# Kernel tuning notes

Hardware: AMD Instinct MI355X
Metric: run time of the kernel (lower is better)

## Reference

```python
import jax, jax.numpy as jnp
import numpy as np

D = 512      # d_model
H = 8        # n_heads
HD = D // H  # head_dim
WIN = 128    # local window
CB = 8       # chunk base
NL = 3       # hierarchy levels
DFF = 1536
B, S = 4, 4096
EPS = 1e-6


def setup_inputs() -> dict:
    key = jax.random.key(0)
    ks = jax.random.split(key, 12)
    sd = 0.02
    inp = {
        'x': jax.random.normal(ks[0], (B, S, D), jnp.float32),
        'norm1_w': jnp.ones((D,), jnp.float32),
        'norm2_w': jnp.ones((D,), jnp.float32),
        'wq': jax.random.normal(ks[1], (D, D), jnp.float32) * sd,
        'wk': jax.random.normal(ks[2], (D, D), jnp.float32) * sd,
        'wv': jax.random.normal(ks[3], (D, D), jnp.float32) * sd,
        'wo': jax.random.normal(ks[4], (D, D), jnp.float32) * sd,
        'gamma': jnp.full((NL,), 0.1, jnp.float32),
        'w1': jax.random.normal(ks[5], (D, DFF), jnp.float32) * sd,
        'w2': jax.random.normal(ks[6], (D, DFF), jnp.float32) * sd,
        'w3': jax.random.normal(ks[7], (DFF, D), jnp.float32) * sd,
    }
    return inp


def rmsnorm(x, w):
    return x * jax.lax.rsqrt(jnp.mean(x * x, axis=-1, keepdims=True) + EPS) * w


def hier_attn(x, wq, wk, wv, wo, gamma):
    b, s, _ = x.shape
    scale = HD ** -0.5
    q = (x @ wq).reshape(b, s, H, HD).transpose(0, 2, 1, 3)  # (b,H,s,hd)
    k = (x @ wk).reshape(b, s, H, HD).transpose(0, 2, 1, 3)
    v = (x @ wv).reshape(b, s, H, HD).transpose(0, 2, 1, 3)

    nb = s // WIN
    qb = q.reshape(b, H, nb, WIN, HD)
    kp = jnp.concatenate([jnp.zeros_like(k[:, :, :WIN]), k], axis=2).reshape(b, H, nb + 1, WIN, HD)
    vp = jnp.concatenate([jnp.zeros_like(v[:, :, :WIN]), v], axis=2).reshape(b, H, nb + 1, WIN, HD)
    kw = jnp.concatenate([kp[:, :, :-1], kp[:, :, 1:]], axis=3)  # (b,H,nb,2W,hd)
    vw = jnp.concatenate([vp[:, :, :-1], vp[:, :, 1:]], axis=3)
    sc = jnp.einsum('bhnqd,bhnkd->bhnqk', qb, kw) * scale
    a_ = jnp.arange(WIN)[:, None]
    j_ = jnp.arange(2 * WIN)[None, :]
    base = (j_ > a_) & (j_ <= a_ + WIN)
    blk = (jnp.arange(nb)[:, None, None] > 0) | (j_ >= WIN)  # first block has no left half
    mask = base[None] & blk                                  # (nb,W,2W)
    sc = jnp.where(mask[None, None], sc, -1e9)
    out = jnp.einsum('bhnqk,bhnkd->bhnqd', jax.nn.softmax(sc, axis=-1), vw).reshape(b, H, s, HD)

    # ---- levels 1..NL: causal attention over mean-pooled chunk summaries ----
    pos = jnp.arange(s)
    for lvl in range(1, NL + 1):
        C = CB ** lvl
        nc = s // C
        kc = k.reshape(b, H, nc, C, HD).mean(axis=3)
        vc = v.reshape(b, H, nc, C, HD).mean(axis=3)
        sl = jnp.einsum('bhsd,bhcd->bhsc', q, kc) * scale
        m = jnp.arange(nc)[None, :] < (pos // C)[:, None]    # chunk strictly in the past
        sl = jnp.where(m[None, None], sl, -1e9)
        p = jax.nn.softmax(sl, axis=-1)
        p = p * m.any(axis=-1)[None, None, :, None]          # zero rows with no valid chunk
        out = out + gamma[lvl - 1] * jnp.einsum('bhsc,bhcd->bhsd', p, vc)

    return out.transpose(0, 2, 1, 3).reshape(b, s, D) @ wo


def swiglu(x, w1, w2, w3):
    return (jax.nn.silu(x @ w1) * (x @ w2)) @ w3


def reference(x, norm1_w, norm2_w, wq, wk, wv, wo, gamma, w1, w2, w3):
    h = x + hier_attn(rmsnorm(x, norm1_w), wq, wk, wv, wo, gamma)
    return h + swiglu(rmsnorm(h, norm2_w), w1, w2, w3)
```

## Files before the change

### kernel.cpp

```cpp
#include <hip/hip_runtime.h>
#include <stdint.h>

typedef unsigned short US;
typedef __attribute__((ext_vector_type(8))) short short8;
typedef __attribute__((ext_vector_type(8))) US us8;
typedef __attribute__((ext_vector_type(4))) float f32x4;
typedef __attribute__((ext_vector_type(4))) int i32x4;

#define DEV static __device__ __forceinline__

DEV US f2b(float f){
  uint32_t u = __builtin_bit_cast(uint32_t, f);
  return (US)((u + 0x7fffu + ((u >> 16) & 1u)) >> 16);
}
DEV US f2b_fast(float f){
  uint32_t u = __builtin_bit_cast(uint32_t, f);
  return (US)((u + 0x8000u) >> 16);
}
DEV float b2f(US s){
  return __builtin_bit_cast(float, (uint32_t)((uint32_t)s << 16));
}
DEV short8 ldsfrag(const US* p){
  return __builtin_bit_cast(short8, *(const i32x4*)p);
}
DEV f32x4 MFMA(short8 a, short8 b, f32x4 c){
  return __builtin_amdgcn_mfma_f32_16x16x32_bf16(a, b, c, 0, 0, 0);
}
DEV void async16(const US* g, US* l){
  __builtin_amdgcn_global_load_lds(
      (const __attribute__((address_space(1))) unsigned int*)(const void*)g,
      (__attribute__((address_space(3))) unsigned int*)(void*)l,
      16, 0, 0);
}

struct WcvtArgs {
  const float* src[7];
  US* dst[7];
  int R[7];
  int C[7];
};

__global__ __launch_bounds__(256) void wcvt(WcvtArgs a){
  int z = blockIdx.z;
  int R = a.R[z], C = a.C[z];
  int tc = blockIdx.x*32, tr = blockIdx.y*32;
  if (tc >= C || tr >= R) return;
  __shared__ float T[32][33];
  int tx = threadIdx.x & 31, ty = threadIdx.x >> 5;
  const float* s = a.src[z];
  #pragma unroll
  for (int j=0;j<4;++j) T[ty + j*8][tx] = s[(size_t)(tr + ty + j*8)*C + tc + tx];
  __syncthreads();
  US* d = a.dst[z];
  #pragma unroll
  for (int j=0;j<4;++j) d[(size_t)(tc + ty + j*8)*R + tr + tx] = f2b(T[tx][ty + j*8]);
}

__global__ __launch_bounds__(256) void rmsnorm_k(const float* __restrict__ x,
                                                 const float* __restrict__ w,
                                                 US* __restrict__ o){
  int row = blockIdx.x*4 + (threadIdx.x >> 6);
  int l = threadIdx.x & 63;
  const float* xr = x + (size_t)row*512 + l*8;
  f32x4 a = *(const f32x4*)xr;
  f32x4 b = *(const f32x4*)(xr + 4);
  float ss = a[0]*a[0]+a[1]*a[1]+a[2]*a[2]+a[3]*a[3]
           + b[0]*b[0]+b[1]*b[1]+b[2]*b[2]+b[3]*b[3];
  #pragma unroll
  for (int mk=1; mk<64; mk<<=1) ss += __shfl_xor(ss, mk);
  float r = rsqrtf(ss*(1.0f/512.0f) + 1e-6f);
  const float* wr = w + l*8;
  f32x4 wa = *(const f32x4*)wr;
  f32x4 wb = *(const f32x4*)(wr + 4);
  us8 t;
  t[0]=f2b(a[0]*r*wa[0]); t[1]=f2b(a[1]*r*wa[1]);
  t[2]=f2b(a[2]*r*wa[2]); t[3]=f2b(a[3]*r*wa[3]);
  t[4]=f2b(b[0]*r*wb[0]); t[5]=f2b(b[1]*r*wb[1]);
  t[6]=f2b(b[2]*r*wb[2]); t[7]=f2b(b[3]*r*wb[3]);
  *(us8*)(o + (size_t)row*512 + l*8) = t;
}

template<int EPI>
__global__ __launch_bounds__(256) void gemm_bt(
    const US* __restrict__ A, const US* __restrict__ BT,
    int M, int N, int K,
    void* __restrict__ outp, const float* __restrict__ auxf,
    US* __restrict__ auxb)
{
  __shared__ __attribute__((aligned(16))) US As[128*64];
  __shared__ __attribute__((aligned(16))) US Bs[128*64];
  const int tid = threadIdx.x, l = tid & 63, w = tid >> 6;
  const int wr = w >> 1, wc = w & 1;
  const int gx = gridDim.x;
  int wg = blockIdx.y*gx + blockIdx.x;
  const int nwg = gx * gridDim.y;
  const int qq = nwg >> 3;
  wg = (wg & 7)*qq + (wg >> 3);
  const int m0 = (wg / gx)*128, n0 = (wg % gx)*128;
  (void)M;
  f32x4 acc[4][4] = {};
  for (int k0 = 0; k0 < K; k0 += 64){
    #pragma unroll
    for (int p=0;p<4;++p){
      int off  = p*4096 + w*1024 + l*16;
      int row  = off >> 7;
      int slot = (off >> 4) & 7;
      int ce   = ((slot ^ (row & 7)) << 3);
      async16(A  + (size_t)(m0 + row)*K + k0 + ce, As + p*2048 + w*512);
      async16(BT + (size_t)(n0 + row)*K + k0 + ce, Bs + p*2048 + w*512);
    }
    __syncthreads();
    short8 af[2][4], bg[2][4];
    #pragma unroll
    for (int kk=0;kk<2;++kk){
      const int sA = ((kk*4 + (l>>4)) ^ (l & 7)) << 3;
      #pragma unroll
      for (int i=0;i<4;++i){
        af[kk][i] = ldsfrag(&As[(wr*64 + i*16 + (l&15))*64 + sA]);
        bg[kk][i] = ldsfrag(&Bs[(wc*64 + i*16 + (l&15))*64 + sA]);
      }
    }
    #pragma unroll
    for (int kk=0;kk<2;++kk)
      #pragma unroll
      for (int i=0;i<4;++i)
        #pragma unroll
        for (int j=0;j<4;++j)
          acc[i][j] = MFMA(af[kk][i], bg[kk][j], acc[i][j]);
    __syncthreads();
  }
  #pragma unroll
  for (int i=0;i<4;++i)
    #pragma unroll
    for (int j=0;j<4;++j)
      #pragma unroll
      for (int r=0;r<4;++r){
        int m  = m0 + wr*64 + i*16 + (l>>4)*4 + r;
        int nn = n0 + wc*64 + j*16 + (l&15);
        float val = acc[i][j][r];
        if constexpr (EPI == 0){
          US* o = (US*)outp;
          int f = nn & 511, t = nn >> 9;
          size_t idx = (size_t)t*8388608
                     + ((size_t)(m>>12)*8 + (size_t)(f>>6))*262144
                     + (size_t)(m & 4095)*64 + (size_t)(f & 63);
          o[idx] = f2b(val);
        } else if constexpr (EPI == 1){
          float* o = (float*)outp;
          size_t idx = (size_t)m*N + nn;
          o[idx] = auxf[idx] + val;
        } else if constexpr (EPI == 2){
          US* o = (US*)outp;
          o[(size_t)m*N + nn] = f2b(val);
        } else {
          float* o = (float*)outp;
          size_t idx = (size_t)m*N + nn;
          o[idx] += val;
        }
      }
  (void)auxb;
}

__global__ __launch_bounds__(256, 2) void gemm_ff12(
    const US* __restrict__ A, const US* __restrict__ B1T, const US* __restrict__ B2T,
    int N, int K, US* __restrict__ outp)
{
  __shared__ __attribute__((aligned(16))) US As[128*64];
  __shared__ __attribute__((aligned(16))) US B1s[128*64];
  __shared__ __attribute__((aligned(16))) US B2s[128*64];
  const int tid = threadIdx.x, l = tid & 63, w = tid >> 6;
  const int wr = w >> 1, wc = w & 1;
  const int gx = gridDim.x;
  int wg = blockIdx.y*gx + blockIdx.x;
  const int nwg = gx * gridDim.y;
  const int qq = nwg >> 3;
  wg = (wg & 7)*qq + (wg >> 3);
  const int m0 = (wg / gx)*128, n0 = (wg % gx)*128;
  f32x4 acc1[4][4] = {};
  f32x4 acc2[4][4] = {};
  for (int k0 = 0; k0 < K; k0 += 64){
    #pragma unroll
    for (int p=0;p<4;++p){
      int off  = p*4096 + w*1024 + l*16;
      int row  = off >> 7;
      int slot = (off >> 4) & 7;
      int ce   = ((slot ^ (row & 7)) << 3);
      async16(A   + (size_t)(m0 + row)*K + k0 + ce, As  + p*2048 + w*512);
      async16(B1T + (size_t)(n0 + row)*K + k0 + ce, B1s + p*2048 + w*512);
      async16(B2T + (size_t)(n0 + row)*K + k0 + ce, B2s + p*2048 + w*512);
    }
    __syncthreads();
    short8 af[2][4], bg1[2][4], bg2[2][4];
    #pragma unroll
    for (int kk=0;kk<2;++kk){
      const int sA = ((kk*4 + (l>>4)) ^ (l & 7)) << 3;
      #pragma unroll
      for (int i=0;i<4;++i){
        af[kk][i]  = ldsfrag(&As [(wr*64 + i*16 + (l&15))*64 + sA]);
        bg1[kk][i] = ldsfrag(&B1s[(wc*64 + i*16 + (l&15))*64 + sA]);
        bg2[kk][i] = ldsfrag(&B2s[(wc*64 + i*16 + (l&15))*64 + sA]);
      }
    }
    #pragma unroll
    for (int kk=0;kk<2;++kk)
      #pragma unroll
      for (int i=0;i<4;++i)
        #pragma unroll
        for (int j=0;j<4;++j){
          acc1[i][j] = MFMA(af[kk][i], bg1[kk][j], acc1[i][j]);
          acc2[i][j] = MFMA(af[kk][i], bg2[kk][j], acc2[i][j]);
        }
    __syncthreads();
  }
  #pragma unroll
  for (int i=0;i<4;++i)
    #pragma unroll
    for (int j=0;j<4;++j)
      #pragma unroll
      for (int r=0;r<4;++r){
        int m  = m0 + wr*64 + i*16 + (l>>4)*4 + r;
        int nn = n0 + wc*64 + j*16 + (l&15);
        float g = acc1[i][j][r];
        float u = acc2[i][j][r];
        float sg = g / (1.f + __expf(-g));
        outp[(size_t)m*N + nn] = f2b(sg * u);
      }
}

__global__ __launch_bounds__(256) void vtrans(const US* __restrict__ vin,
                                              US* __restrict__ vout){
  __shared__ US T[64*72];
  int s0 = blockIdx.x*64;
  int bh = blockIdx.y;
  int r = threadIdx.x >> 2, c0 = (threadIdx.x & 3)*16;
  const US* src = vin + ((size_t)bh*4096 + s0 + r)*64 + c0;
  *(i32x4*)&T[r*72 + c0]     = *(const i32x4*)src;
  *(i32x4*)&T[r*72 + c0 + 8] = *(const i32x4*)(src + 8);
  __syncthreads();
  int d = threadIdx.x >> 2, e0 = (threadIdx.x & 3)*16;
  US* dst = vout + ((size_t)bh*64 + d)*4096 + s0 + e0;
  us8 o0, o1;
  #pragma unroll
  for (int j=0;j<8;++j){ o0[j] = T[(e0+j)*72 + d]; o1[j] = T[(e0+8+j)*72 + d]; }
  *(us8*)dst = o0;
  *(us8*)(dst + 8) = o1;
}

__global__ __launch_bounds__(256) void poolkvt(
    const US* __restrict__ kin, US* __restrict__ kout,
    const US* __restrict__ vtin, US* __restrict__ vtout,
    int nin, int nout, int lgno, int noutS, int lgnoS)
{
  int t = blockIdx.x*256 + threadIdx.x;
  if (blockIdx.y == 0){
    if (t >= (nout << 11)) return;
    int d = t & 63;
    int c = (t >> 6) & (nout - 1);
    int bh = t >> (6 + lgno);
    const US* kp = kin + (((size_t)bh*nin) + (size_t)c*8)*64 + d;
    float s = 0.f;
    #pragma unroll
    for (int j=0;j<8;++j) s += b2f(kp[j*64]);
    kout[((size_t)bh*nout + c)*64 + d] = f2b(s*0.125f);
  } else {
    if (t >= (noutS << 11)) return;
    int c = t & (noutS - 1);
    int row = t >> lgnoS;
    US val = 0;
    if (c < nout){
      const US* vp = vtin + (size_t)row*nin + (size_t)c*8;
      us8 v = *(const us8*)vp;
      float s = 0.f;
      #pragma unroll
      for (int j=0;j<8;++j) s += b2f(v[j]);
      val = f2b(s*0.125f);
    }
    vtout[(size_t)row*noutS + c] = val;
  }
}

template<int NFV, bool LOCAL>
DEV void flash_level(const US* __restrict__ kptr, const US* __restrict__ vtp,
                     int vstride, int ncK, int NCV,
                     int tile0, int ntiles, int lg,
                     int tid, int l, int w, int prow,
                     short8 aq0, short8 aq1,
                     US* Ks, US* Vs, US* Ps,
                     float* lsum, f32x4* olvl)
{
  for (int tt=0; tt<ntiles; ++tt){
    const int cb = (tile0 + tt)*128;
    __syncthreads();
    {
      int r = tid >> 2, c0 = (tid & 3)*16;
      if (cb + r < ncK){
        const US* kp = kptr + (size_t)(cb + r)*64 + c0;
        *(i32x4*)&Ks[r*72 + c0]     = *(const i32x4*)kp;
        *(i32x4*)&Ks[r*72 + c0 + 8] = *(const i32x4*)(kp + 8);
      }
      int d = tid >> 3, e0 = (tid & 7)*16;
      US* dst = &Vs[d*136 + e0];
      if (cb + e0 + 16 <= NCV){
        const US* vp = vtp + (size_t)d*vstride + cb + e0;
        *(i32x4*)dst       = *(const i32x4*)vp;
        *(i32x4*)(dst + 8) = *(const i32x4*)(vp + 8);
      } else {
        i32x4 z = {0,0,0,0};
        *(i32x4*)dst = z; *(i32x4*)(dst + 8) = z;
      }
    }
    __syncthreads();
    f32x4 sc[NFV];
    #pragma unroll
    for (int nf=0; nf<NFV; ++nf){
      const US* kb_ = &Ks[(nf*16 + (l&15))*72 + (l>>4)*8];
      f32x4 z = {0.f,0.f,0.f,0.f};
      z = MFMA(aq0, ldsfrag(kb_), z);
      sc[nf] = MFMA(aq1, ldsfrag(kb_ + 32), z);
    }
    #pragma unroll
    for (int nf=0; nf<NFV; ++nf){
      int c = cb + nf*16 + (l&15);
      #pragma unroll
      for (int i=0;i<4;++i){
        int p = prow + i;
        bool valid = LOCAL ? (c >= p - 127 && c <= p) : (c < (p >> lg));
        sc[nf][i] = valid ? sc[nf][i]*0.125f : -1e30f;
      }
    }
    #pragma unroll
    for (int i=0;i<4;++i){
      float rs = 0.f;
      #pragma unroll
      for (int nf=0; nf<NFV; ++nf){ float e = __expf(sc[nf][i]); sc[nf][i] = e; rs += e; }
      #pragma unroll
      for (int mk=1; mk<16; mk<<=1) rs += __shfl_xor(rs, mk);
      lsum[i] += rs;
    }
    #pragma unroll
    for (int nf=0; nf<NFV; ++nf)
      #pragma unroll
      for (int i=0;i<4;++i)
        Ps[w*2176 + ((l>>4)*4 + i)*136 + nf*16 + (l&15)] = f2b_fast(sc[nf][i]);
    #pragma unroll
    for (int kf=0; kf<NFV/2; ++kf){
      short8 pa = ldsfrag(&Ps[w*2176 + (l&15)*136 + kf*32 + (l>>4)*8]);
      #pragma unroll
      for (int df=0; df<4; ++df){
        short8 vb_ = ldsfrag(&Vs[(df*16 + (l&15))*136 + kf*32 + (l>>4)*8]);
        olvl[df] = MFMA(pa, vb_, olvl[df]);
      }
    }
  }
}

__global__ __launch_bounds__(512, 4) void attn_fused(
    const US* __restrict__ q, const US* __restrict__ k, const US* __restrict__ vt,
    const US* __restrict__ kc1, const US* __restrict__ vc1t,
    const US* __restrict__ kc2, const US* __restrict__ vc2t,
    const US* __restrict__ kc3, const US* __restrict__ vc3t,
    const float* __restrict__ gamma, US* __restrict__ ao)
{
  __shared__ __attribute__((aligned(16))) US Ks[128*72];
  __shared__ __attribute__((aligned(16))) US Vs[64*136];
  __shared__ __attribute__((aligned(16))) US Ps[8*16*136];
  const int nblk = blockIdx.x, h = blockIdx.y, b = blockIdx.z;
  const int tid = threadIdx.x, l = tid & 63, w = tid >> 6;
  const int bh = b*8 + h;
  const int prow = nblk*128 + w*16 + ((l>>4)<<2);
  short8 aq0, aq1;
  {
    int s = nblk*128 + w*16 + (l & 15);
    const US* qp = q + ((size_t)bh*4096 + s)*64 + (l >> 4)*8;
    aq0 = __builtin_bit_cast(short8, *(const i32x4*)qp);
    aq1 = __builtin_bit_cast(short8, *(const i32x4*)(qp + 32));
  }
  float lsum[4];
  f32x4 olvl[4], oacc[4];
  #pragma unroll
  for (int i=0;i<4;++i) oacc[i] = (f32x4){0.f,0.f,0.f,0.f};

  #pragma unroll
  for (int i=0;i<4;++i){ lsum[i]=0.f; olvl[i]=(f32x4){0.f,0.f,0.f,0.f}; }
  flash_level<8,true>(k + (size_t)bh*262144, vt + (size_t)bh*262144, 4096, 4096, 4096,
                      (nblk>0)?(nblk-1):0, (nblk>0)?2:1, 0,
                      tid,l,w,prow,aq0,aq1,Ks,Vs,Ps,lsum,olvl);
  #pragma unroll
  for (int i=0;i<4;++i){
    float wgt = 1.f/lsum[i];
    #pragma unroll
    for (int df=0;df<4;++df) oacc[df][i] += olvl[df][i]*wgt;
  }

  const float g0 = gamma[0], g1 = gamma[1], g2 = gamma[2];

  #pragma unroll
  for (int i=0;i<4;++i){ lsum[i]=0.f; olvl[i]=(f32x4){0.f,0.f,0.f,0.f}; }
  {
    int cme = (nblk*128 + 127) >> 3;
    int nt = (cme + 127) >> 7;
    flash_level<8,false>(kc1 + (size_t)bh*32768, vc1t + (size_t)bh*32768, 512, 512, 512,
                         0, nt, 3, tid,l,w,prow,aq0,aq1,Ks,Vs,Ps,lsum,olvl);
  }
  #pragma unroll
  for (int i=0;i<4;++i){
    if (prow + i >= 8){
      float wgt = g0/lsum[i];
      #pragma unroll
      for (int df=0;df<4;++df) oacc[df][i] += olvl[df][i]*wgt;
    }
  }

  #pragma unroll
  for (int i=0;i<4;++i){ lsum[i]=0.f; olvl[i]=(f32x4){0.f,0.f,0.f,0.f}; }
  flash_level<4,false>(kc2 + (size_t)bh*4096, vc2t + (size_t)bh*4096, 64, 64, 64,
                       0, 1, 6, tid,l,w,prow,aq0,aq1,Ks,Vs,Ps,lsum,olvl);
  #pragma unroll
  for (int i=0;i<4;++i){
    if (prow + i >= 64){
      float wgt = g1/lsum[i];
      #pragma unroll
      for (int df=0;df<4;++df) oacc[df][i] += olvl[df][i]*wgt;
    }
  }

  if (nblk >= 4){
    #pragma unroll
    for (int i=0;i<4;++i){ lsum[i]=0.f; olvl[i]=(f32x4){0.f,0.f,0.f,0.f}; }
    flash_level<2,false>(kc3 + (size_t)bh*512, vc3t + (size_t)bh*1024, 16, 8, 16,
                         0, 1, 9, tid,l,w,prow,aq0,aq1,Ks,Vs,Ps,lsum,olvl);
    #pragma unroll
    for (int i=0;i<4;++i){
      if (prow + i >= 512){
        float wgt = g2/lsum[i];
        #pragma unroll
        for (int df=0;df<4;++df) oacc[df][i] += olvl[df][i]*wgt;
      }
    }
  }

  #pragma unroll
  for (int df=0;df<4;++df)
    #pragma unroll
    for (int i=0;i<4;++i){
      int p = prow + i, d = df*16 + (l&15);
      ao[((size_t)b*4096 + p)*512 + h*64 + d] = f2b(oacc[df][i]);
    }
}

static constexpr size_t SZ_WT_SQ = (size_t)512*512*2;
static constexpr size_t SZ_WT_FF = (size_t)512*1536*2;
static constexpr size_t SZ_ACT   = (size_t)16384*512*2;
static constexpr size_t O_WQT = 0;
static constexpr size_t O_WKT = O_WQT + SZ_WT_SQ;
static constexpr size_t O_WVT = O_WKT + SZ_WT_SQ;
static constexpr size_t O_WOT = O_WVT + SZ_WT_SQ;
static constexpr size_t O_W1T = O_WOT + SZ_WT_SQ;
static constexpr size_t O_W2T = O_W1T + SZ_WT_FF;
static constexpr size_t O_W3T = O_W2T + SZ_WT_FF;
static constexpr size_t O_XN  = O_W3T + SZ_WT_FF;
static constexpr size_t O_Q   = O_XN + SZ_ACT;
static constexpr size_t O_K   = O_Q + SZ_ACT;
static constexpr size_t O_V   = O_K + SZ_ACT;
static constexpr size_t O_AO  = O_V + SZ_ACT;
static constexpr size_t O_KC1 = O_AO + SZ_ACT;
static constexpr size_t O_VC1T = O_KC1 + (size_t)32*512*64*2;
static constexpr size_t O_KC2  = O_VC1T + (size_t)32*64*512*2;
static constexpr size_t O_VC2T = O_KC2 + (size_t)32*64*64*2;
static constexpr size_t O_KC3  = O_VC2T + (size_t)32*64*64*2;
static constexpr size_t O_VC3T = O_KC3 + (size_t)32*8*64*2;

extern "C" void kernel_launch(void* const* d_in, const int* in_sizes, int n_in,
                              void* d_out, int out_size, void* d_ws, size_t ws_size,
                              hipStream_t stream)
{
  (void)in_sizes; (void)n_in; (void)out_size; (void)ws_size;
  const float* x     = (const float*)d_in[0];
  const float* n1w   = (const float*)d_in[1];
  const float* n2w   = (const float*)d_in[2];
  const float* wq    = (const float*)d_in[3];
  const float* wk    = (const float*)d_in[4];
  const float* wv    = (const float*)d_in[5];
  const float* wo    = (const float*)d_in[6];
  const float* gamma = (const float*)d_in[7];
  const float* w1    = (const float*)d_in[8];
  const float* w2    = (const float*)d_in[9];
  const float* w3    = (const float*)d_in[10];
  float* out = (float*)d_out;
  char* ws = (char*)d_ws;

  US* wqT = (US*)(ws + O_WQT);
  US* wkT = (US*)(ws + O_WKT);
  US* wvT = (US*)(ws + O_WVT);
  US* woT = (US*)(ws + O_WOT);
  US* w1T = (US*)(ws + O_W1T);
  US* w2T = (US*)(ws + O_W2T);
  US* w3T = (US*)(ws + O_W3T);
  US* xn  = (US*)(ws + O_XN);
  US* qb  = (US*)(ws + O_Q);
  US* kb  = (US*)(ws + O_K);
  US* vb  = (US*)(ws + O_V);
  US* ao  = (US*)(ws + O_AO);
  US* kc1 = (US*)(ws + O_KC1);
  US* vc1t = (US*)(ws + O_VC1T);
  US* kc2  = (US*)(ws + O_KC2);
  US* vc2t = (US*)(ws + O_VC2T);
  US* kc3  = (US*)(ws + O_KC3);
  US* vc3t = (US*)(ws + O_VC3T);
  US* vbt = xn;
  US* up1 = (US*)(ws + O_Q);

  WcvtArgs wa;
  wa.src[0]=wq; wa.dst[0]=wqT; wa.R[0]=512;  wa.C[0]=512;
  wa.src[1]=wk; wa.dst[1]=wkT; wa.R[1]=512;  wa.C[1]=512;
  wa.src[2]=wv; wa.dst[2]=wvT; wa.R[2]=512;  wa.C[2]=512;
  wa.src[3]=wo; wa.dst[3]=woT; wa.R[3]=512;  wa.C[3]=512;
  wa.src[4]=w1; wa.dst[4]=w1T; wa.R[4]=512;  wa.C[4]=1536;
  wa.src[5]=w2; wa.dst[5]=w2T; wa.R[5]=512;  wa.C[5]=1536;
  wa.src[6]=w3; wa.dst[6]=w3T; wa.R[6]=1536; wa.C[6]=512;
  wcvt<<<dim3(48,48,7), 256, 0, stream>>>(wa);

  rmsnorm_k<<<dim3(4096), 256, 0, stream>>>(x, n1w, xn);

  gemm_bt<0><<<dim3(12,128), 256, 0, stream>>>(xn, wqT, 16384,1536,512, (void*)qb, nullptr, nullptr);

  vtrans<<<dim3(64,32), 256, 0, stream>>>(vb, vbt);

  poolkvt<<<dim3(4096,2), 256, 0, stream>>>(kb,  kc1, vbt,  vc1t, 4096, 512, 9, 512, 9);
  poolkvt<<<dim3(512,2),  256, 0, stream>>>(kc1, kc2, vc1t, vc2t, 512,  64,  6, 64,  6);
  poolkvt<<<dim3(128,2),  256, 0, stream>>>(kc2, kc3, vc2t, vc3t, 64,   8,   3, 16,  4);

  attn_fused<<<dim3(32,8,4), 512, 0, stream>>>(qb, kb, vbt, kc1, vc1t, kc2, vc2t, kc3, vc3t, gamma, ao);

  gemm_bt<1><<<dim3(4,128), 256, 0, stream>>>(ao, woT, 16384,512,512, (void*)out, x, nullptr);

  rmsnorm_k<<<dim3(4096), 256, 0, stream>>>(out, n2w, xn);

  gemm_ff12<<<dim3(12,128), 256, 0, stream>>>(xn, w1T, w2T, 1536, 512, up1);

  gemm_bt<4><<<dim3(4,128), 256, 0, stream>>>(up1, w3T, 16384,512,1536, (void*)out, nullptr, nullptr);
}
```

Measured before the change: 272.2 us.

## Use 512-thread FFN gate GEMM and async swizzled K/V tile loads in attention

The fused SwiGLU up-projection GEMM now runs with 8 waves per 128x128 tile instead of 4. Each wave owns a 64x32 sub-tile, which halves its accumulator registers, and LDS fragments are loaded per k-step instead of all up front. In the attention kernel, K and V^T tiles are now brought into LDS with async global-to-LDS copies using an XOR-swizzled layout rather than padded rows loaded through registers. This shrinks LDS use but drops the explicit zero-fill of out-of-range V columns, which relies on those entries being masked or harmless.

```diff
diff --git a/kernel.cpp b/kernel.cpp
--- a/kernel.cpp
+++ b/kernel.cpp
@@ -161,7 +161,7 @@
   (void)auxb;
 }
 
-__global__ __launch_bounds__(256, 2) void gemm_ff12(
+__global__ __launch_bounds__(512) void gemm_ff12(
     const US* __restrict__ A, const US* __restrict__ B1T, const US* __restrict__ B2T,
     int N, int K, US* __restrict__ outp)
 {
@@ -169,57 +169,61 @@
   __shared__ __attribute__((aligned(16))) US B1s[128*64];
   __shared__ __attribute__((aligned(16))) US B2s[128*64];
   const int tid = threadIdx.x, l = tid & 63, w = tid >> 6;
-  const int wr = w >> 1, wc = w & 1;
+  const int wr = w >> 2, wc = w & 3;
   const int gx = gridDim.x;
   int wg = blockIdx.y*gx + blockIdx.x;
   const int nwg = gx * gridDim.y;
   const int qq = nwg >> 3;
   wg = (wg & 7)*qq + (wg >> 3);
   const int m0 = (wg / gx)*128, n0 = (wg % gx)*128;
-  f32x4 acc1[4][4] = {};
-  f32x4 acc2[4][4] = {};
+  f32x4 acc1[4][2] = {};
+  f32x4 acc2[4][2] = {};
   for (int k0 = 0; k0 < K; k0 += 64){
     #pragma unroll
-    for (int p=0;p<4;++p){
-      int off  = p*4096 + w*1024 + l*16;
+    for (int p=0;p<2;++p){
+      int off  = p*8192 + tid*16;
       int row  = off >> 7;
       int slot = (off >> 4) & 7;
       int ce   = ((slot ^ (row & 7)) << 3);
-      async16(A   + (size_t)(m0 + row)*K + k0 + ce, As  + p*2048 + w*512);
-      async16(B1T + (size_t)(n0 + row)*K + k0 + ce, B1s + p*2048 + w*512);
-      async16(B2T + (size_t)(n0 + row)*K + k0 + ce, B2s + p*2048 + w*512);
+      async16(A   + (size_t)(m0 + row)*K + k0 + ce, As  + p*4096 + w*512);
+      async16(B1T + (size_t)(n0 + row)*K + k0 + ce, B1s + p*4096 + w*512);
+      async16(B2T + (size_t)(n0 + row)*K + k0 + ce, B2s + p*4096 + w*512);
     }
     __syncthreads();
-    short8 af[2][4], bg1[2][4], bg2[2][4];
     #pragma unroll
     for (int kk=0;kk<2;++kk){
-      const int sA = ((kk*4 + (l>>4)) ^ (l & 7)) << 3;
+      short8 af[4], b1[2], b2[2];
       #pragma unroll
       for (int i=0;i<4;++i){
-        af[kk][i]  = ldsfrag(&As [(wr*64 + i*16 + (l&15))*64 + sA]);
-        bg1[kk][i] = ldsfrag(&B1s[(wc*64 + i*16 + (l&15))*64 + sA]);
-        bg2[kk][i] = ldsfrag(&B2s[(wc*64 + i*16 + (l&15))*64 + sA]);
-      }
-    }
-    #pragma unroll
-    for (int kk=0;kk<2;++kk)
+        int row = wr*64 + i*16 + (l&15);
+        int s = ((kk*4 + (l>>4)) ^ (row & 7)) << 3;
+        af[i] = ldsfrag(&As[row*64 + s]);
+      }
+      #pragma unroll
+      for (int j=0;j<2;++j){
+        int row = wc*32 + j*16 + (l&15);
+        int s = ((kk*4 + (l>>4)) ^ (row & 7)) << 3;
+        b1[j] = ldsfrag(&B1s[row*64 + s]);
+        b2[j] = ldsfrag(&B2s[row*64 + s]);
+      }
       #pragma unroll
       for (int i=0;i<4;++i)
         #pragma unroll
-        for (int j=0;j<4;++j){
-          acc1[i][j] = MFMA(af[kk][i], bg1[kk][j], acc1[i][j]);
-          acc2[i][j] = MFMA(af[kk][i], bg2[kk][j], acc2[i][j]);
+        for (int j=0;j<2;++j){
+          acc1[i][j] = MFMA(af[i], b1[j], acc1[i][j]);
+          acc2[i][j] = MFMA(af[i], b2[j], acc2[i][j]);
         }
+    }
     __syncthreads();
   }
   #pragma unroll
   for (int i=0;i<4;++i)
     #pragma unroll
-    for (int j=0;j<4;++j)
+    for (int j=0;j<2;++j)
       #pragma unroll
       for (int r=0;r<4;++r){
         int m  = m0 + wr*64 + i*16 + (l>>4)*4 + r;
-        int nn = n0 + wc*64 + j*16 + (l&15);
+        int nn = n0 + wc*32 + j*16 + (l&15);
         float g = acc1[i][j][r];
         float u = acc2[i][j][r];
         float sg = g / (1.f + __expf(-g));
@@ -291,32 +295,34 @@
   for (int tt=0; tt<ntiles; ++tt){
     const int cb = (tile0 + tt)*128;
     __syncthreads();
-    {
-      int r = tid >> 2, c0 = (tid & 3)*16;
-      if (cb + r < ncK){
-        const US* kp = kptr + (size_t)(cb + r)*64 + c0;
-        *(i32x4*)&Ks[r*72 + c0]     = *(const i32x4*)kp;
-        *(i32x4*)&Ks[r*72 + c0 + 8] = *(const i32x4*)(kp + 8);
-      }
-      int d = tid >> 3, e0 = (tid & 7)*16;
-      US* dst = &Vs[d*136 + e0];
-      if (cb + e0 + 16 <= NCV){
-        const US* vp = vtp + (size_t)d*vstride + cb + e0;
-        *(i32x4*)dst       = *(const i32x4*)vp;
-        *(i32x4*)(dst + 8) = *(const i32x4*)(vp + 8);
-      } else {
-        i32x4 z = {0,0,0,0};
-        *(i32x4*)dst = z; *(i32x4*)(dst + 8) = z;
+    #pragma unroll
+    for (int is=0; is<2; ++is){
+      int off  = is*8192 + tid*16;
+      {
+        int row  = off >> 7;
+        int slot = (off >> 4) & 7;
+        int ce   = ((slot ^ (row & 7)) << 3);
+        if (cb + row < ncK)
+          async16(kptr + (size_t)(cb + row)*64 + ce, Ks + is*4096 + w*512);
+      }
+      {
+        int row = off >> 8;
+        int q   = ((off >> 4) & 15) ^ (row & 7);
+        if (cb + q*8 < NCV)
+          async16(vtp + (size_t)row*vstride + cb + q*8, Vs + is*4096 + w*512);
       }
     }
     __syncthreads();
     f32x4 sc[NFV];
     #pragma unroll
     for (int nf=0; nf<NFV; ++nf){
-      const US* kb_ = &Ks[(nf*16 + (l&15))*72 + (l>>4)*8];
+      int row = nf*16 + (l&15);
+      const US* base = &Ks[row*64];
+      int s0 = (((l>>4)    ) ^ (row & 7)) << 3;
+      int s1 = (((l>>4) + 4) ^ (row & 7)) << 3;
       f32x4 z = {0.f,0.f,0.f,0.f};
-      z = MFMA(aq0, ldsfrag(kb_), z);
-      sc[nf] = MFMA(aq1, ldsfrag(kb_ + 32), z);
+      z = MFMA(aq0, ldsfrag(base + s0), z);
+      sc[nf] = MFMA(aq1, ldsfrag(base + s1), z);
     }
     #pragma unroll
     for (int nf=0; nf<NFV; ++nf){
@@ -347,7 +353,9 @@
       short8 pa = ldsfrag(&Ps[w*2176 + (l&15)*136 + kf*32 + (l>>4)*8]);
       #pragma unroll
       for (int df=0; df<4; ++df){
-        short8 vb_ = ldsfrag(&Vs[(df*16 + (l&15))*136 + kf*32 + (l>>4)*8]);
+        int row = df*16 + (l&15);
+        int s = ((kf*4 + (l>>4)) ^ (row & 7)) << 3;
+        short8 vb_ = ldsfrag(&Vs[row*128 + s]);
         olvl[df] = MFMA(pa, vb_, olvl[df]);
       }
     }
@@ -361,8 +369,8 @@
     const US* __restrict__ kc3, const US* __restrict__ vc3t,
     const float* __restrict__ gamma, US* __restrict__ ao)
 {
-  __shared__ __attribute__((aligned(16))) US Ks[128*72];
-  __shared__ __attribute__((aligned(16))) US Vs[64*136];
+  __shared__ __attribute__((aligned(16))) US Ks[128*64];
+  __shared__ __attribute__((aligned(16))) US Vs[64*128];
   __shared__ __attribute__((aligned(16))) US Ps[8*16*136];
   const int nblk = blockIdx.x, h = blockIdx.y, b = blockIdx.z;
   const int tid = threadIdx.x, l = tid & 63, w = tid >> 6;
@@ -536,7 +544,7 @@
 
   rmsnorm_k<<<dim3(4096), 256, 0, stream>>>(out, n2w, xn);
 
-  gemm_ff12<<<dim3(12,128), 256, 0, stream>>>(xn, w1T, w2T, 1536, 512, up1);
+  gemm_ff12<<<dim3(12,128), 512, 0, stream>>>(xn, w1T, w2T, 1536, 512, up1);
 
   gemm_bt<4><<<dim3(4,128), 256, 0, stream>>>(up1, w3T, 16384,512,1536, (void*)out, nullptr, nullptr);
 }
```

Result: no change. 269.7 us (-0.9%).
